# Kernel optimization log

Hardware: AMD Instinct MI355X
Metric: run time of the kernel (lower is better)

Reference implementation:

```python
import jax, jax.numpy as jnp
import numpy as np

EPS = 0.1
MAX_ITER = 100
THRESH = 0.1


def setup_inputs() -> dict:
    key = jax.random.key(0)
    k1, k2 = jax.random.split(key)
    N = 4096
    x = jax.random.normal(k1, (N, N), dtype=jnp.float32)
    y = jax.random.normal(k2, (N, N), dtype=jnp.float32)
    return {"x": x, "y": y}


def _sinkhorn(x, y):
    # forward softmaxes inputs along last dim
    x = jax.nn.softmax(x, axis=-1)
    y = jax.nn.softmax(y, axis=-1)
    # squared-euclidean cost |x_i - y_j|^2, expanded to avoid an [N,N,D] broadcast
    x2 = jnp.sum(x * x, axis=-1)  # [n]
    y2 = jnp.sum(y * y, axis=-1)  # [m]
    C = x2[:, None] + y2[None, :] - 2.0 * (x @ y.T)  # [n, m]
    n = x.shape[-1]  # source sizes mu/nu by the FEATURE dim (requires n == m == d)
    log_mu = jnp.log(jnp.full((n,), 1.0 / n, dtype=C.dtype) + 1e-8)
    log_nu = log_mu

    def M(u, v):
        # faithful to source: both u and v broadcast over the COLUMN axis
        return (-C + u[None, :] + v[None, :]) / EPS

    def step(carry, _):
        u, v, done = carry
        u1 = u
        u_new = EPS * (log_mu - jax.nn.logsumexp(M(u, v), axis=-1)) + u
        v_new = EPS * (log_nu - jax.nn.logsumexp(M(u_new, v).T, axis=-1)) + v
        # torch: (u-u1).abs().sum(-1).mean() with implicit batch of 1 == plain sum
        err = jnp.sum(jnp.abs(u_new - u1))
        u = jnp.where(done, u, u_new)
        v = jnp.where(done, v, v_new)
        return (u, v, done | (err < THRESH)), None

    init = (jnp.zeros((n,), C.dtype), jnp.zeros((n,), C.dtype), jnp.array(False))
    (u, v, _), _ = jax.lax.scan(step, init, None, length=MAX_ITER)
    pi = jnp.exp(M(u, v))  # [n, m] (torch returns [1, n, m]; batch dim squeezed)
    cost = jnp.sum(pi * C)  # cost.mean() over the singleton batch == scalar sum
    return cost, pi, C


def reference(x, y):
    return _sinkhorn(x, y)
```

## Files before the change

### kernel.cpp

```cpp
#include <hip/hip_runtime.h>
#include <math.h>

#define NN 4096
#define KTILES 64

typedef __bf16 bf16;
typedef __attribute__((ext_vector_type(4))) __bf16 bf16x4;
typedef __attribute__((ext_vector_type(8))) __bf16 bf16x8;
typedef __attribute__((ext_vector_type(4))) float f32x4;

#define MFMA16(a, b, c) __builtin_amdgcn_mfma_f32_16x16x32_bf16((a), (b), (c), 0, 0, 0)

__device__ __forceinline__ void gld16(const void* g, void* l) {
  __builtin_amdgcn_global_load_lds((const __attribute__((address_space(1))) void*)g,
                                   (__attribute__((address_space(3))) void*)l, 16, 0, 0);
}


__device__ __forceinline__ double blockSumD(double v) {
  __shared__ double w[4];
  #pragma unroll
  for (int o = 32; o > 0; o >>= 1) v += __shfl_down(v, o, 64);
  __syncthreads();
  if ((threadIdx.x & 63) == 0) w[threadIdx.x >> 6] = v;
  __syncthreads();
  return w[0] + w[1] + w[2] + w[3];
}

__device__ __forceinline__ float blockMaxF(float v) {
  __shared__ float w[4];
  #pragma unroll
  for (int o = 32; o > 0; o >>= 1) v = fmaxf(v, __shfl_down(v, o, 64));
  __syncthreads();
  if ((threadIdx.x & 63) == 0) w[threadIdx.x >> 6] = v;
  __syncthreads();
  return fmaxf(fmaxf(w[0], w[1]), fmaxf(w[2], w[3]));
}


__global__ void softmax_rows(const float* __restrict__ x, const float* __restrict__ y,
                             bf16* __restrict__ xh, bf16* __restrict__ yh,
                             float* __restrict__ rowsq) {
  int row = blockIdx.x;
  int r = (row < NN) ? row : row - NN;
  const f32x4* __restrict__ src = (const f32x4*)(((row < NN) ? x : y) + (size_t)r * NN);
  bf16x4* __restrict__ dst = (bf16x4*)(((row < NN) ? xh : yh) + (size_t)r * NN);
  int t = threadIdx.x;

  f32x4 v[4];
  float m = -3.402823466e38f;
  #pragma unroll
  for (int j = 0; j < 4; ++j) {
    v[j] = src[t + 256 * j];
    m = fmaxf(fmaxf(fmaxf(m, v[j].x), fmaxf(v[j].y, v[j].z)), v[j].w);
  }
  float M = blockMaxF(m);

  float s = 0.0f;
  #pragma unroll
  for (int j = 0; j < 4; ++j) {
    v[j].x = expf(v[j].x - M); v[j].y = expf(v[j].y - M);
    v[j].z = expf(v[j].z - M); v[j].w = expf(v[j].w - M);
    s += (v[j].x + v[j].y) + (v[j].z + v[j].w);
  }
  double S = blockSumD((double)s);
  float inv = (float)(1.0 / S);

  float q = 0.0f;
  #pragma unroll
  for (int j = 0; j < 4; ++j) {
    f32x4 p = v[j] * inv;
    bf16x4 h;
    h.x = (bf16)p.x; h.y = (bf16)p.y; h.z = (bf16)p.z; h.w = (bf16)p.w;
    dst[t + 256 * j] = h;
    q += (p.x * p.x + p.y * p.y) + (p.z * p.z + p.w * p.w);
  }
  double Q = blockSumD((double)q);
  if (t == 0) rowsq[row] = (float)Q;
}


__global__ __launch_bounds__(512, 2) void gemm_bt(const bf16* __restrict__ A,
                                                  const bf16* __restrict__ B,
                                                  const float* __restrict__ rowsq,
                                                  float* __restrict__ C,
                                                  float* __restrict__ colpart) {
  __shared__ __align__(16) bf16 sm[2][4][8192];
  __shared__ float lsc[2][256];
  char* smb = (char*)sm;

  const int t = threadIdx.x;
  const int i0 = blockIdx.y * 256;
  const int j0 = blockIdx.x * 256;
  const int w = t >> 6, l = t & 63;
  const int wr = w >> 2, wc = w & 3;
  const int lr = l & 15, lq = l >> 4;

  const int c0 = t, c1 = t + 512;
  const int r0 = c0 >> 3, r1 = c1 >> 3;
  const int g0 = ((c0 & 7) ^ (r0 & 7)) * 8;
  const int g1 = ((c1 & 7) ^ (r1 & 7)) * 8;

  const bf16* A0p = A + (size_t)i0 * NN;
  const bf16* A1p = A0p + (size_t)128 * NN;
  const bf16* B0p = B + (size_t)j0 * NN;
  const bf16* B1p = B0p + (size_t)128 * NN;

  const int jx0 = lq ^ (lr & 7);
  const int jx1 = (4 + lq) ^ (lr & 7);
  const int aO0 = lr * 128 + jx0 * 16;
  const int aO1 = lr * 128 + jx1 * 16;
  const int brO = (wc & 1) * 8192;

  f32x4 acc[8][4] = {};

  auto STG = [&](const bf16* gp, char* ld) {
    gld16(gp + (size_t)r0 * NN + g0, ld + c0 * 16);
    gld16(gp + (size_t)r1 * NN + g1, ld + c1 * 16);
  };

  {
    char* s0 = smb;
    char* s1 = smb + 65536;
    STG(B0p, s0 + 32768);
    STG(B1p, s0 + 49152);
    STG(A0p, s0);
    STG(A1p, s0 + 16384);
    STG(B0p + 64, s1 + 32768);
    STG(B1p + 64, s1 + 49152);
    STG(A0p + 64, s1);
  }
  asm volatile("s_waitcnt vmcnt(6)" ::: "memory");
  __builtin_amdgcn_s_barrier();

  #pragma unroll 1
  for (int tt = 0; tt < KTILES; ++tt) {
    const int cur = tt & 1;
    char* baseC = smb + (cur << 16);
    char* baseN = smb + ((cur ^ 1) << 16);
    const char* Arw = baseC + wr * 16384;
    const char* Brw = baseC + 32768 + ((wc >> 1) << 14) + brO;

    bf16x8 bg[4][2], af[4][2];

    #pragma unroll
    for (int jj = 0; jj < 4; ++jj) {
      bg[jj][0] = *(const bf16x8*)(Brw + jj * 2048 + aO0);
      bg[jj][1] = *(const bf16x8*)(Brw + jj * 2048 + aO1);
    }
    #pragma unroll
    for (int i = 0; i < 4; ++i) {
      af[i][0] = *(const bf16x8*)(Arw + i * 2048 + aO0);
      af[i][1] = *(const bf16x8*)(Arw + i * 2048 + aO1);
    }
    if (tt < KTILES - 1) STG(A1p + (tt + 1) * 64, baseN + 16384);
    __builtin_amdgcn_s_barrier();
    asm volatile("s_waitcnt lgkmcnt(0)" ::: "memory");
    __builtin_amdgcn_s_setprio(1);
    #pragma unroll
    for (int i = 0; i < 4; ++i)
      #pragma unroll
      for (int jj = 0; jj < 2; ++jj) {
        acc[i][jj] = MFMA16(af[i][0], bg[jj][0], acc[i][jj]);
        acc[i][jj] = MFMA16(af[i][1], bg[jj][1], acc[i][jj]);
      }
    __builtin_amdgcn_s_setprio(0);
    __builtin_amdgcn_s_barrier();

    if (tt < KTILES - 2) STG(B0p + (tt + 2) * 64, baseC + 32768);
    __builtin_amdgcn_s_barrier();
    __builtin_amdgcn_s_setprio(1);
    #pragma unroll
    for (int i = 0; i < 4; ++i)
      #pragma unroll
      for (int jj = 0; jj < 2; ++jj) {
        acc[i][2 + jj] = MFMA16(af[i][0], bg[2 + jj][0], acc[i][2 + jj]);
        acc[i][2 + jj] = MFMA16(af[i][1], bg[2 + jj][1], acc[i][2 + jj]);
      }
    __builtin_amdgcn_s_setprio(0);
    __builtin_amdgcn_s_barrier();

    #pragma unroll
    for (int i = 0; i < 4; ++i) {
      af[i][0] = *(const bf16x8*)(Arw + 8192 + i * 2048 + aO0);
      af[i][1] = *(const bf16x8*)(Arw + 8192 + i * 2048 + aO1);
    }
    if (tt < KTILES - 2) STG(B1p + (tt + 2) * 64, baseC + 49152);
    __builtin_amdgcn_s_barrier();
    asm volatile("s_waitcnt lgkmcnt(0)" ::: "memory");
    __builtin_amdgcn_s_setprio(1);
    #pragma unroll
    for (int i = 0; i < 4; ++i)
      #pragma unroll
      for (int jj = 0; jj < 2; ++jj) {
        acc[4 + i][2 + jj] = MFMA16(af[i][0], bg[2 + jj][0], acc[4 + i][2 + jj]);
        acc[4 + i][2 + jj] = MFMA16(af[i][1], bg[2 + jj][1], acc[4 + i][2 + jj]);
      }
    __builtin_amdgcn_s_setprio(0);
    __builtin_amdgcn_s_barrier();

    if (tt < KTILES - 2) {
      STG(A0p + (tt + 2) * 64, baseC);
      asm volatile("s_waitcnt vmcnt(6)" ::: "memory");
    } else if (tt == KTILES - 2) {
      asm volatile("s_waitcnt vmcnt(0)" ::: "memory");
    }
    __builtin_amdgcn_s_barrier();
    __builtin_amdgcn_s_setprio(1);
    #pragma unroll
    for (int i = 0; i < 4; ++i)
      #pragma unroll
      for (int jj = 0; jj < 2; ++jj) {
        acc[4 + i][jj] = MFMA16(af[i][0], bg[jj][0], acc[4 + i][jj]);
        acc[4 + i][jj] = MFMA16(af[i][1], bg[jj][1], acc[4 + i][jj]);
      }
    __builtin_amdgcn_s_setprio(0);
    __builtin_amdgcn_s_barrier();
  }

  float y2v[4], ec[4] = {0.f, 0.f, 0.f, 0.f};
  #pragma unroll
  for (int jj = 0; jj < 4; ++jj) y2v[jj] = rowsq[NN + j0 + wc * 64 + 16 * jj + lr];
  #pragma unroll
  for (int m = 0; m < 8; ++m) {
    #pragma unroll
    for (int r = 0; r < 4; ++r) {
      int grow = i0 + wr * 128 + 16 * m + lq * 4 + r;
      float x2 = rowsq[grow];
      size_t rowoff = (size_t)grow * NN + j0 + wc * 64;
      #pragma unroll
      for (int jj = 0; jj < 4; ++jj) {
        float cv = x2 + y2v[jj] - 2.0f * acc[m][jj][r];
        C[rowoff + 16 * jj + lr] = cv;
        ec[jj] += expf(-10.0f * cv);
      }
    }
  }
  #pragma unroll
  for (int jj = 0; jj < 4; ++jj) {
    ec[jj] += __shfl_xor(ec[jj], 16, 64);
    ec[jj] += __shfl_xor(ec[jj], 32, 64);
  }
  if (lq == 0) {
    #pragma unroll
    for (int jj = 0; jj < 4; ++jj) lsc[wr][wc * 64 + 16 * jj + lr] = ec[jj];
  }
  __syncthreads();
  if (t < 256) colpart[(size_t)blockIdx.y * NN + j0 + t] = lsc[0][t] + lsc[1][t];
}


__global__ void col_lse_final(const float* __restrict__ colpart, float* __restrict__ sdf) {
  int col = blockIdx.x * 256 + threadIdx.x;
  double s = 0.0;
  #pragma unroll
  for (int ch = 0; ch < 16; ++ch) s += (double)colpart[(size_t)ch * NN + col];
  double log_nu = log(1.0 / (double)NN + 1e-8);
  sdf[col] = (float)(log_nu - log(s));
}


__global__ void pi_cost(const float* __restrict__ Cm, const float* __restrict__ sdf,
                        float* __restrict__ pi, double* __restrict__ costpart) {
  size_t idx0 = (size_t)blockIdx.x * 2048 + threadIdx.x;
  float facc = 0.0f;
  #pragma unroll
  for (int j = 0; j < 8; ++j) {
    size_t idx = idx0 + 256 * j;
    float c = Cm[idx];
    int col = (int)(idx & (NN - 1));
    float p = expf(fmaf(-10.0f, c, sdf[col]));
    pi[idx] = p;
    facc = fmaf(p, c, facc);
  }
  double total = blockSumD((double)facc);
  if (threadIdx.x == 0) costpart[blockIdx.x] = total;
}


__global__ void cost_final(const double* __restrict__ costpart, float* __restrict__ out) {
  double s = 0.0;
  #pragma unroll
  for (int j = 0; j < 32; ++j) s += costpart[threadIdx.x + 256 * j];
  double total = blockSumD(s);
  if (threadIdx.x == 0) out[0] = (float)total;
}


extern "C" void kernel_launch(void* const* d_in, const int* in_sizes, int n_in,
                              void* d_out, int out_size, void* d_ws, size_t ws_size,
                              hipStream_t stream) {
  const float* x = (const float*)d_in[0];
  const float* y = (const float*)d_in[1];
  float* out = (float*)d_out;
  float* pi = out + 1;
  float* Cm = out + 1 + (size_t)NN * NN;

  char* ws = (char*)d_ws;
  bf16* xh = (bf16*)ws;
  bf16* yh = xh + (size_t)NN * NN;
  size_t off = (size_t)NN * NN * 2 * 2;
  float* rowsq = (float*)(ws + off);       off += 2 * NN * 4;
  float* sdf = (float*)(ws + off);         off += NN * 4;
  float* colpart = (float*)(ws + off);     off += 32 * NN * 4;
  double* costpart = (double*)(ws + off);  off += 8192 * 8;

  hipLaunchKernelGGL(softmax_rows, dim3(2 * NN), dim3(256), 0, stream, x, y, xh, yh, rowsq);
  hipLaunchKernelGGL(gemm_bt, dim3(16, 16), dim3(512), 0, stream, xh, yh, rowsq, Cm, colpart);
  hipLaunchKernelGGL(col_lse_final, dim3(16), dim3(256), 0, stream, colpart, sdf);
  hipLaunchKernelGGL(pi_cost, dim3(8192), dim3(256), 0, stream, Cm, sdf, pi, costpart);
  hipLaunchKernelGGL(cost_final, dim3(1), dim3(256), 0, stream, costpart, out);
}
```

Before: 366.3 us.

## Software-pipeline LDS fragment loads across GEMM k-tiles with split lo/hi registers

Restructures the MFMA main loop so the A-low and B-low fragments for the next k-tile are read from LDS at the end of the current iteration. The first MFMA phase can then start without waiting on LDS reads, and the B-high reads overlap it via a partial lgkmcnt wait. The quadrant order of MFMA phases is changed so each fragment set is consumed just after it arrives. This adds register pressure from keeping separate lo/hi fragment arrays, which could lower occupancy or cause spills.

```diff
diff --git a/kernel.cpp b/kernel.cpp
--- a/kernel.cpp
+++ b/kernel.cpp
@@ -113,6 +113,7 @@
   const int brO = (wc & 1) * 8192;
 
   f32x4 acc[8][4] = {};
+  bf16x8 alo[4][2], ahi[4][2], blo[2][2], bhi[2][2];
 
   auto STG = [&](const bf16* gp, char* ld) {
     gld16(gp + (size_t)r0 * NN + g0, ld + c0 * 16);
@@ -132,6 +133,20 @@
   }
   asm volatile("s_waitcnt vmcnt(6)" ::: "memory");
   __builtin_amdgcn_s_barrier();
+  {
+    const char* Arw = smb + wr * 16384;
+    const char* Brw = smb + 32768 + ((wc >> 1) << 14) + brO;
+    #pragma unroll
+    for (int i = 0; i < 4; ++i) {
+      alo[i][0] = *(const bf16x8*)(Arw + i * 2048 + aO0);
+      alo[i][1] = *(const bf16x8*)(Arw + i * 2048 + aO1);
+    }
+    #pragma unroll
+    for (int jj = 0; jj < 2; ++jj) {
+      blo[jj][0] = *(const bf16x8*)(Brw + jj * 2048 + aO0);
+      blo[jj][1] = *(const bf16x8*)(Brw + jj * 2048 + aO1);
+    }
+  }
 
   #pragma unroll 1
   for (int tt = 0; tt < KTILES; ++tt) {
@@ -140,20 +155,29 @@
     char* baseN = smb + ((cur ^ 1) << 16);
     const char* Arw = baseC + wr * 16384;
     const char* Brw = baseC + 32768 + ((wc >> 1) << 14) + brO;
-
-    bf16x8 bg[4][2], af[4][2];
-
-    #pragma unroll
-    for (int jj = 0; jj < 4; ++jj) {
-      bg[jj][0] = *(const bf16x8*)(Brw + jj * 2048 + aO0);
-      bg[jj][1] = *(const bf16x8*)(Brw + jj * 2048 + aO1);
-    }
-    #pragma unroll
-    for (int i = 0; i < 4; ++i) {
-      af[i][0] = *(const bf16x8*)(Arw + i * 2048 + aO0);
-      af[i][1] = *(const bf16x8*)(Arw + i * 2048 + aO1);
+    const char* ArwN = baseN + wr * 16384;
+    const char* BrwN = baseN + 32768 + ((wc >> 1) << 14) + brO;
+
+    #pragma unroll
+    for (int jj = 0; jj < 2; ++jj) {
+      bhi[jj][0] = *(const bf16x8*)(Brw + (2 + jj) * 2048 + aO0);
+      bhi[jj][1] = *(const bf16x8*)(Brw + (2 + jj) * 2048 + aO1);
     }
     if (tt < KTILES - 1) STG(A1p + (tt + 1) * 64, baseN + 16384);
+    __builtin_amdgcn_s_barrier();
+    asm volatile("s_waitcnt lgkmcnt(4)" ::: "memory");
+    __builtin_amdgcn_s_setprio(1);
+    #pragma unroll
+    for (int i = 0; i < 4; ++i)
+      #pragma unroll
+      for (int jj = 0; jj < 2; ++jj) {
+        acc[i][jj] = MFMA16(alo[i][0], blo[jj][0], acc[i][jj]);
+        acc[i][jj] = MFMA16(alo[i][1], blo[jj][1], acc[i][jj]);
+      }
+    __builtin_amdgcn_s_setprio(0);
+    __builtin_amdgcn_s_barrier();
+
+    if (tt < KTILES - 2) STG(B0p + (tt + 2) * 64, baseC + 32768);
     __builtin_amdgcn_s_barrier();
     asm volatile("s_waitcnt lgkmcnt(0)" ::: "memory");
     __builtin_amdgcn_s_setprio(1);
@@ -161,29 +185,16 @@
     for (int i = 0; i < 4; ++i)
       #pragma unroll
       for (int jj = 0; jj < 2; ++jj) {
-        acc[i][jj] = MFMA16(af[i][0], bg[jj][0], acc[i][jj]);
-        acc[i][jj] = MFMA16(af[i][1], bg[jj][1], acc[i][jj]);
+        acc[i][2 + jj] = MFMA16(alo[i][0], bhi[jj][0], acc[i][2 + jj]);
+        acc[i][2 + jj] = MFMA16(alo[i][1], bhi[jj][1], acc[i][2 + jj]);
       }
     __builtin_amdgcn_s_setprio(0);
     __builtin_amdgcn_s_barrier();
 
-    if (tt < KTILES - 2) STG(B0p + (tt + 2) * 64, baseC + 32768);
-    __builtin_amdgcn_s_barrier();
-    __builtin_amdgcn_s_setprio(1);
-    #pragma unroll
-    for (int i = 0; i < 4; ++i)
-      #pragma unroll
-      for (int jj = 0; jj < 2; ++jj) {
-        acc[i][2 + jj] = MFMA16(af[i][0], bg[2 + jj][0], acc[i][2 + jj]);
-        acc[i][2 + jj] = MFMA16(af[i][1], bg[2 + jj][1], acc[i][2 + jj]);
-      }
-    __builtin_amdgcn_s_setprio(0);
-    __builtin_amdgcn_s_barrier();
-
     #pragma unroll
     for (int i = 0; i < 4; ++i) {
-      af[i][0] = *(const bf16x8*)(Arw + 8192 + i * 2048 + aO0);
-      af[i][1] = *(const bf16x8*)(Arw + 8192 + i * 2048 + aO1);
+      ahi[i][0] = *(const bf16x8*)(Arw + 8192 + i * 2048 + aO0);
+      ahi[i][1] = *(const bf16x8*)(Arw + 8192 + i * 2048 + aO1);
     }
     if (tt < KTILES - 2) STG(B1p + (tt + 2) * 64, baseC + 49152);
     __builtin_amdgcn_s_barrier();
@@ -193,8 +204,8 @@
     for (int i = 0; i < 4; ++i)
       #pragma unroll
       for (int jj = 0; jj < 2; ++jj) {
-        acc[4 + i][2 + jj] = MFMA16(af[i][0], bg[2 + jj][0], acc[4 + i][2 + jj]);
-        acc[4 + i][2 + jj] = MFMA16(af[i][1], bg[2 + jj][1], acc[4 + i][2 + jj]);
+        acc[4 + i][jj] = MFMA16(ahi[i][0], blo[jj][0], acc[4 + i][jj]);
+        acc[4 + i][jj] = MFMA16(ahi[i][1], blo[jj][1], acc[4 + i][jj]);
       }
     __builtin_amdgcn_s_setprio(0);
     __builtin_amdgcn_s_barrier();
@@ -211,10 +222,23 @@
     for (int i = 0; i < 4; ++i)
       #pragma unroll
       for (int jj = 0; jj < 2; ++jj) {
-        acc[4 + i][jj] = MFMA16(af[i][0], bg[jj][0], acc[4 + i][jj]);
-        acc[4 + i][jj] = MFMA16(af[i][1], bg[jj][1], acc[4 + i][jj]);
+        acc[4 + i][2 + jj] = MFMA16(ahi[i][0], bhi[jj][0], acc[4 + i][2 + jj]);
+        acc[4 + i][2 + jj] = MFMA16(ahi[i][1], bhi[jj][1], acc[4 + i][2 + jj]);
       }
     __builtin_amdgcn_s_setprio(0);
+    __builtin_amdgcn_sched_barrier(0);
+    if (tt < KTILES - 1) {
+      #pragma unroll
+      for (int i = 0; i < 4; ++i) {
+        alo[i][0] = *(const bf16x8*)(ArwN + i * 2048 + aO0);
+        alo[i][1] = *(const bf16x8*)(ArwN + i * 2048 + aO1);
+      }
+      #pragma unroll
+      for (int jj = 0; jj < 2; ++jj) {
+        blo[jj][0] = *(const bf16x8*)(BrwN + jj * 2048 + aO0);
+        blo[jj][1] = *(const bf16x8*)(BrwN + jj * 2048 + aO1);
+      }
+    }
     __builtin_amdgcn_s_barrier();
   }
 
```

Measured after the change: 368.2 us. No clear change (+0.5%).
